# Performance work log

Hardware: AMD Instinct MI355X
Metric: run time of the kernel (lower is better)

The kernel has to match this reference:

```python
import jax, jax.numpy as jnp
import numpy as np
from jax import lax

B, S, H, W = 64, 256, 512, 512


def _lstm_cell(x_t, h, c, Wih, Whh, bih, bhh):
    # PyTorch LSTMCell gate order: i, f, g, o
    g = x_t @ Wih.T + h @ Whh.T + bih + bhh  # [B, 4H]
    i, f, gg, o = jnp.split(g, 4, axis=-1)
    c_new = jax.nn.sigmoid(f) * c + jax.nn.sigmoid(i) * jnp.tanh(gg)
    h_new = jax.nn.sigmoid(o) * jnp.tanh(c_new)
    return h_new, c_new


def setup_inputs() -> dict:
    key = jax.random.key(0)
    ks = jax.random.split(key, 12)
    bnd = 1.0 / np.sqrt(H)
    u = lambda k, shape, b: jax.random.uniform(k, shape, jnp.float32, -b, b)
    return {
        "x": jax.random.normal(ks[0], (B, S, S), jnp.float32),
        "enc_Wih": u(ks[1], (4 * H, S), bnd),
        "enc_Whh": u(ks[2], (4 * H, H), bnd),
        "enc_bih": u(ks[3], (4 * H,), bnd),
        "enc_bhh": u(ks[4], (4 * H,), bnd),
        "dec_Wih": u(ks[5], (4 * H, S), bnd),
        "dec_Whh": u(ks[6], (4 * H, H), bnd),
        "dec_bih": u(ks[7], (4 * H,), bnd),
        "dec_bhh": u(ks[8], (4 * H,), bnd),
        "w1": u(ks[9], (W, H), 1.0 / np.sqrt(H)),
        "w2": u(ks[10], (W, H), 1.0 / np.sqrt(H)),
        "vt": u(ks[11], (W,), 1.0 / np.sqrt(W)),
    }


def reference(x, enc_Wih, enc_Whh, enc_bih, enc_bhh,
              dec_Wih, dec_Whh, dec_bih, dec_bhh, w1, w2, vt):
    xs = x.transpose(1, 0, 2)  # [S, B, S] time-major

    # ---- encoder LSTM (zero initial state, PyTorch default) ----
    def enc_step(carry, x_t):
        h, c = carry
        h, c = _lstm_cell(x_t, h, c, enc_Wih, enc_Whh, enc_bih, enc_bhh)
        return (h, c), h

    h0 = jnp.zeros((B, H), x.dtype)
    (hT, cT), enc_out = lax.scan(enc_step, (h0, h0), xs)  # enc_out: [S, B, H]

    # loop-invariant W1 projection of encoder outputs
    e1 = jnp.einsum('sbh,wh->sbw', enc_out, w1)  # [S, B, W]

    # ---- decoder: hidden updates each step; cell stays at cT (faithful to source) ----
    def dec_step(h, x_t):
        h_new, _ = _lstm_cell(x_t, h, cT, dec_Wih, dec_Whh, dec_bih, dec_bhh)
        att = jnp.tanh(e1 + (h_new @ w2.T)[None, :, :])   # [S, B, W]
        scores = jnp.einsum('sbw,w->sb', att, vt)          # [S, B]
        lp = jax.nn.log_softmax(scores.T, axis=-1)         # [B, S]
        return h_new, lp

    _, probs = lax.scan(dec_step, hT, xs)  # [S_dec, B, S]
    return probs.transpose(1, 0, 2)        # [B, S_dec, S]
```

## Files before the change

kernel.cpp:

```cpp
#include <hip/hip_runtime.h>
#include <cmath>

__device__ __forceinline__ float sigm(float x) { return 1.0f / (1.0f + __expf(-x)); }

__global__ __launch_bounds__(256) void transpose_w(const float* __restrict__ in,
                                                   float* __restrict__ outT, int K) {
  __shared__ float tile[32][33];
  int tx = threadIdx.x & 31, ty = threadIdx.x >> 5;
  int k0 = blockIdx.x * 32;
  int j0 = blockIdx.y * 32;
#pragma unroll
  for (int i = 0; i < 32; i += 8)
    tile[ty + i][tx] = in[(size_t)(j0 + ty + i) * K + k0 + tx];
  __syncthreads();
#pragma unroll
  for (int i = 0; i < 32; i += 8)
    outT[(size_t)(k0 + ty + i) * 2048 + j0 + tx] = tile[tx][ty + i];
}

__device__ __forceinline__ void gemv_j(const float4* __restrict__ A4,
                                       const float4* __restrict__ W4, int j, int kqx,
                                       int kq, int jlo, int jhi, int b0, int b1,
                                       float (&o0)[8], float (&o1)[8]) {
  int qa = (j << 3) + kqx;
  float4 a04 = A4[b0 * 192 + qa];
  float4 a14 = A4[b1 * 192 + qa];
  int wr = ((j << 3) + kq) << 2;
  float a0v[4] = {a04.x, a04.y, a04.z, a04.w};
  float a1v[4] = {a14.x, a14.y, a14.z, a14.w};
#pragma unroll
  for (int i = 0; i < 4; ++i) {
    float4 wlo = W4[(wr + i) * 8 + jlo];
    float4 whi = W4[(wr + i) * 8 + jhi];
    o0[0] = fmaf(a0v[i], wlo.x, o0[0]);
    o0[1] = fmaf(a0v[i], wlo.y, o0[1]);
    o0[2] = fmaf(a0v[i], wlo.z, o0[2]);
    o0[3] = fmaf(a0v[i], wlo.w, o0[3]);
    o0[4] = fmaf(a0v[i], whi.x, o0[4]);
    o0[5] = fmaf(a0v[i], whi.y, o0[5]);
    o0[6] = fmaf(a0v[i], whi.z, o0[6]);
    o0[7] = fmaf(a0v[i], whi.w, o0[7]);
    o1[0] = fmaf(a1v[i], wlo.x, o1[0]);
    o1[1] = fmaf(a1v[i], wlo.y, o1[1]);
    o1[2] = fmaf(a1v[i], wlo.z, o1[2]);
    o1[3] = fmaf(a1v[i], wlo.w, o1[3]);
    o1[4] = fmaf(a1v[i], whi.x, o1[4]);
    o1[5] = fmaf(a1v[i], whi.y, o1[5]);
    o1[6] = fmaf(a1v[i], whi.z, o1[6]);
    o1[7] = fmaf(a1v[i], whi.w, o1[7]);
  }
}

__global__ __launch_bounds__(256, 1) void lstm_chain(
    const float* __restrict__ WT, const float* __restrict__ x,
    const float* __restrict__ bih, const float* __restrict__ bhh,
    float* __restrict__ HBUF,
    float* __restrict__ Cst,
    unsigned int* __restrict__ flg,
    int is_enc) {
  extern __shared__ float lds[];
  float4* W4 = (float4*)lds;
  float4* A4 = (float4*)(lds + 24576);
  float* gates = lds + 24576 + 12288;
  const int bg = blockIdx.x >> 6, ng = blockIdx.x & 63;
  const int tid = threadIdx.x;
  unsigned int* myflag = flg + (size_t)(bg * 64 + ng) * 32;
  unsigned int* dom = flg + (size_t)bg * 64 * 32;

#pragma unroll
  for (int r = 0; r < 24; ++r) {
    int idx = tid + 256 * r;
    int k = idx >> 3, j = idx & 7;
    float4 v =
        *(const float4*)(WT + (size_t)k * 2048 + (j >> 1) * 512 + ng * 8 + (j & 1) * 4);
    W4[k * 8 + (j ^ ((k >> 2) & 7))] = v;
  }
  float bi_i = 0.f, bi_f = 0.f, bi_g = 0.f, bi_o = 0.f, creg = 0.f;
  if (tid < 128) {
    int b = tid >> 3, n8 = tid & 7;
    int n_g = ng * 8 + n8;
    bi_i = bih[n_g] + bhh[n_g];
    bi_f = bih[512 + n_g] + bhh[512 + n_g];
    bi_g = bih[1024 + n_g] + bhh[1024 + n_g];
    bi_o = bih[1536 + n_g] + bhh[1536 + n_g];
    if (!is_enc) creg = Cst[(size_t)(bg * 16 + b) * 512 + n_g];
  }
#pragma unroll
  for (int r = 0; r < 8; ++r) {
    int idx = tid + 256 * r;
    int b = idx >> 7, q = idx & 127;
    float4 v;
    if (is_enc)
      v = make_float4(0.f, 0.f, 0.f, 0.f);
    else
      v = *(const float4*)(HBUF + ((size_t)(255 * 64) + bg * 16 + b) * 512 + 4 * q);
    A4[b * 192 + (q ^ ((b >> 1) & 7))] = v;
  }
#pragma unroll
  for (int r = 0; r < 4; ++r) {
    int idx = tid + 256 * r;
    int b = idx >> 6, q = idx & 63;
    float4 v = *(const float4*)(x + ((size_t)(bg * 16 + b) * 256 + 0) * 256 + 4 * q);
    A4[b * 192 + ((128 + q) ^ ((b >> 1) & 7))] = v;
  }
  __syncthreads();

  const int w = tid >> 6;
  const int lane = tid & 63;
  const int kq = lane >> 3, b8 = lane & 7;
  const int b0 = 2 * b8, b1 = b0 + 1;
  const int jlo = (2 * w) ^ kq, jhi = (2 * w + 1) ^ kq;
  const int kqx = kq ^ b8;

  for (int t = 0; t < 256; ++t) {
    float acc0[8], acc1[8];
#pragma unroll
    for (int g = 0; g < 8; ++g) { acc0[g] = 0.f; acc1[g] = 0.f; }
#pragma unroll 2
    for (int j = 0; j < 24; ++j)
      gemv_j(A4, W4, j, kqx, kq, jlo, jhi, b0, b1, acc0, acc1);
#pragma unroll
    for (int d = 8; d <= 32; d <<= 1) {
#pragma unroll
      for (int g = 0; g < 8; ++g) {
        acc0[g] += __shfl_xor(acc0[g], d, 64);
        acc1[g] += __shfl_xor(acc1[g], d, 64);
      }
    }
    if (kq == 0) {
#pragma unroll
      for (int g = 0; g < 8; ++g) {
        gates[b0 * 40 + w * 8 + g] = acc0[g];
        gates[b1 * 40 + w * 8 + g] = acc1[g];
      }
    }
    __syncthreads();
    if (tid < 128) {
      int b = tid >> 3, n8 = tid & 7;
      float pi = gates[b * 40 + n8] + bi_i;
      float pf = gates[b * 40 + 8 + n8] + bi_f;
      float pg = gates[b * 40 + 16 + n8] + bi_g;
      float po = gates[b * 40 + 24 + n8] + bi_o;
      float ig = sigm(pi), fg = sigm(pf), gg = tanhf(pg), og = sigm(po);
      float cn = fmaf(fg, creg, ig * gg);
      if (is_enc) creg = cn;
      float hn = og * tanhf(cn);
      float* hp = HBUF + ((size_t)t * 64 + bg * 16 + b) * 512 + ng * 8 + n8;
      __hip_atomic_store(hp, hn, __ATOMIC_RELAXED, __HIP_MEMORY_SCOPE_AGENT);
      if (is_enc && t == 255) Cst[(size_t)(bg * 16 + b) * 512 + ng * 8 + n8] = cn;
    }
    if (t == 255) break;
    asm volatile("s_waitcnt vmcnt(0)" ::: "memory");
    __syncthreads();
    if (tid == 0)
      __hip_atomic_store(myflag, (unsigned)(t + 1), __ATOMIC_RELAXED,
                         __HIP_MEMORY_SCOPE_AGENT);
    asm volatile("" ::: "memory");
#pragma unroll
    for (int r = 0; r < 4; ++r) {
      int idx = tid + 256 * r;
      int b = idx >> 6, q = idx & 63;
      float4 v =
          *(const float4*)(x + ((size_t)(bg * 16 + b) * 256 + (t + 1)) * 256 + 4 * q);
      A4[b * 192 + ((128 + q) ^ ((b >> 1) & 7))] = v;
    }
    if (tid < 64) {
      const unsigned tgt = (unsigned)(t + 1);
      unsigned int* fp = dom + (size_t)tid * 32;
      while (true) {
        unsigned v = __hip_atomic_load(fp, __ATOMIC_RELAXED, __HIP_MEMORY_SCOPE_AGENT);
        if (__all((int)(v >= tgt))) break;
        __builtin_amdgcn_s_sleep(1);
      }
    }
    __syncthreads();
    const float4* hb = (const float4*)(HBUF + (size_t)t * 64 * 512);
#pragma unroll
    for (int r = 0; r < 8; ++r) {
      int idx = tid + 256 * r;
      int b = idx >> 7, q = idx & 127;
      float4 v = hb[(size_t)(bg * 16 + b) * 128 + q];
      A4[b * 192 + (q ^ ((b >> 1) & 7))] = v;
    }
    __syncthreads();
  }
}

__global__ __launch_bounds__(256) void gemm_fp32(const float* __restrict__ A,
                                                 const float* __restrict__ W,
                                                 float* __restrict__ C, int N, int K) {
  __shared__ float As[16 * 132];
  __shared__ float Ws[16 * 132];
  int tid = threadIdx.x;
  int n0 = blockIdx.x * 128, m0 = blockIdx.y * 128;
  int row = tid >> 1;
  int kbase = (tid & 1) * 8;
  const float* ap = A + (size_t)(m0 + row) * K;
  const float* wp = W + (size_t)(n0 + row) * K;
  int ty = tid >> 4, tx = tid & 15;
  float acc[8][8];
#pragma unroll
  for (int i = 0; i < 8; ++i)
#pragma unroll
    for (int j = 0; j < 8; ++j) acc[i][j] = 0.f;

  for (int kt = 0; kt < K; kt += 16) {
    float4 va0 = *(const float4*)(ap + kt + kbase);
    float4 va1 = *(const float4*)(ap + kt + kbase + 4);
    float4 vw0 = *(const float4*)(wp + kt + kbase);
    float4 vw1 = *(const float4*)(wp + kt + kbase + 4);
    __syncthreads();
    As[(kbase + 0) * 132 + row] = va0.x;
    As[(kbase + 1) * 132 + row] = va0.y;
    As[(kbase + 2) * 132 + row] = va0.z;
    As[(kbase + 3) * 132 + row] = va0.w;
    As[(kbase + 4) * 132 + row] = va1.x;
    As[(kbase + 5) * 132 + row] = va1.y;
    As[(kbase + 6) * 132 + row] = va1.z;
    As[(kbase + 7) * 132 + row] = va1.w;
    Ws[(kbase + 0) * 132 + row] = vw0.x;
    Ws[(kbase + 1) * 132 + row] = vw0.y;
    Ws[(kbase + 2) * 132 + row] = vw0.z;
    Ws[(kbase + 3) * 132 + row] = vw0.w;
    Ws[(kbase + 4) * 132 + row] = vw1.x;
    Ws[(kbase + 5) * 132 + row] = vw1.y;
    Ws[(kbase + 6) * 132 + row] = vw1.z;
    Ws[(kbase + 7) * 132 + row] = vw1.w;
    __syncthreads();
#pragma unroll
    for (int kk = 0; kk < 16; ++kk) {
      float4 a0 = *(const float4*)&As[kk * 132 + ty * 8];
      float4 a1 = *(const float4*)&As[kk * 132 + ty * 8 + 4];
      float4 w0 = *(const float4*)&Ws[kk * 132 + tx * 8];
      float4 w1 = *(const float4*)&Ws[kk * 132 + tx * 8 + 4];
      float av[8] = {a0.x, a0.y, a0.z, a0.w, a1.x, a1.y, a1.z, a1.w};
      float wv[8] = {w0.x, w0.y, w0.z, w0.w, w1.x, w1.y, w1.z, w1.w};
#pragma unroll
      for (int i = 0; i < 8; ++i)
#pragma unroll
        for (int j = 0; j < 8; ++j) acc[i][j] = fmaf(av[i], wv[j], acc[i][j]);
    }
  }
#pragma unroll
  for (int i = 0; i < 8; ++i) {
    float* cp = C + (size_t)(m0 + ty * 8 + i) * N + n0 + tx * 8;
    *(float4*)cp = make_float4(acc[i][0], acc[i][1], acc[i][2], acc[i][3]);
    *(float4*)(cp + 4) = make_float4(acc[i][4], acc[i][5], acc[i][6], acc[i][7]);
  }
}

__global__ __launch_bounds__(256) void scorer(const float* __restrict__ E1,
                                              const float* __restrict__ H2,
                                              const float* __restrict__ vt,
                                              float* __restrict__ out) {
  extern __shared__ float smem[];
  float* e1s = smem;
  float* h2s = smem + 8256;
  int tid = threadIdx.x;
  int sx = blockIdx.x;
  int b = blockIdx.y;
#pragma unroll
  for (int j = 0; j < 8; ++j) {
    int idx = tid + 256 * j;
    int r = idx >> 7, c4 = idx & 127;
    float4 v = *(const float4*)(E1 + ((size_t)(sx * 16 + r) * 64 + b) * 512 + c4 * 4);
    *(float4*)&e1s[r * 516 + c4 * 4] = v;
  }
  int tl = tid >> 4, sl = tid & 15;
  for (int tt = 0; tt < 16; ++tt) {
    __syncthreads();
#pragma unroll
    for (int j = 0; j < 8; ++j) {
      int idx = tid + 256 * j;
      int r = idx >> 7, c4 = idx & 127;
      float4 v = *(const float4*)(H2 + ((size_t)(tt * 16 + r) * 64 + b) * 512 + c4 * 4);
      *(float4*)&h2s[r * 516 + c4 * 4] = v;
    }
    __syncthreads();
    float acc = 0.f;
    const float* ep = &e1s[sl * 516];
    const float* hp = &h2s[tl * 516];
#pragma unroll 8
    for (int w4 = 0; w4 < 128; ++w4) {
      float4 a = *(const float4*)(ep + w4 * 4);
      float4 h = *(const float4*)(hp + w4 * 4);
      float4 vv = *(const float4*)(vt + w4 * 4);
      float x0 = a.x + h.x, x1 = a.y + h.y, x2 = a.z + h.z, x3 = a.w + h.w;
      float t0 = fmaf(-2.f, __builtin_amdgcn_rcpf(__expf(x0 + x0) + 1.f), 1.f);
      float t1 = fmaf(-2.f, __builtin_amdgcn_rcpf(__expf(x1 + x1) + 1.f), 1.f);
      float t2 = fmaf(-2.f, __builtin_amdgcn_rcpf(__expf(x2 + x2) + 1.f), 1.f);
      float t3 = fmaf(-2.f, __builtin_amdgcn_rcpf(__expf(x3 + x3) + 1.f), 1.f);
      acc = fmaf(t0, vv.x, acc);
      acc = fmaf(t1, vv.y, acc);
      acc = fmaf(t2, vv.z, acc);
      acc = fmaf(t3, vv.w, acc);
    }
    out[((size_t)b * 256 + tt * 16 + tl) * 256 + sx * 16 + sl] = acc;
  }
}

__global__ __launch_bounds__(256) void logsoftmax_kernel(float* __restrict__ out) {
  __shared__ float red[256];
  int tid = threadIdx.x;
  float* row = out + (size_t)blockIdx.x * 256;
  float v = row[tid];
  red[tid] = v;
  __syncthreads();
  for (int off = 128; off > 0; off >>= 1) {
    if (tid < off) red[tid] = fmaxf(red[tid], red[tid + off]);
    __syncthreads();
  }
  float mx = red[0];
  __syncthreads();
  red[tid] = __expf(v - mx);
  __syncthreads();
  for (int off = 128; off > 0; off >>= 1) {
    if (tid < off) red[tid] += red[tid + off];
    __syncthreads();
  }
  float lse = logf(red[0]);
  row[tid] = v - mx - lse;
}

extern "C" void kernel_launch(void* const* d_in, const int* in_sizes, int n_in,
                              void* d_out, int out_size, void* d_ws, size_t ws_size,
                              hipStream_t stream) {
  (void)in_sizes; (void)n_in; (void)out_size; (void)ws_size;
  const float* x = (const float*)d_in[0];
  const float* eWih = (const float*)d_in[1];
  const float* eWhh = (const float*)d_in[2];
  const float* ebih = (const float*)d_in[3];
  const float* ebhh = (const float*)d_in[4];
  const float* dWih = (const float*)d_in[5];
  const float* dWhh = (const float*)d_in[6];
  const float* dbih = (const float*)d_in[7];
  const float* dbhh = (const float*)d_in[8];
  const float* w1 = (const float*)d_in[9];
  const float* w2 = (const float*)d_in[10];
  const float* vt = (const float*)d_in[11];
  float* out = (float*)d_out;
  float* ws = (float*)d_ws;

  float* E1 = ws;
  float* H2 = E1 + 8388608ull;
  float* HBUF = H2 + 8388608ull;
  float* WTe = HBUF + 8388608ull;
  float* WTd = WTe + 1572864ull;
  float* Cst = WTd + 1572864ull;
  unsigned int* FLG = (unsigned int*)(Cst + 32768ull);

  const unsigned ldsB = (24576 + 12288 + 640) * 4;
  const unsigned scorerLds = 2 * 16 * 516 * 4;

  hipMemsetAsync(FLG, 0, 16384 * sizeof(unsigned int), stream);
  transpose_w<<<dim3(16, 64), 256, 0, stream>>>(eWhh, WTe, 512);
  transpose_w<<<dim3(8, 64), 256, 0, stream>>>(eWih, WTe + 512 * 2048, 256);
  transpose_w<<<dim3(16, 64), 256, 0, stream>>>(dWhh, WTd, 512);
  transpose_w<<<dim3(8, 64), 256, 0, stream>>>(dWih, WTd + 512 * 2048, 256);

  {
    const float* a0 = WTe; const float* a1 = x; const float* a2 = ebih;
    const float* a3 = ebhh; float* a4 = HBUF; float* a5 = Cst;
    unsigned int* a6 = FLG; int a7 = 1;
    void* args[] = {&a0, &a1, &a2, &a3, &a4, &a5, &a6, &a7};
    hipLaunchCooperativeKernel((const void*)lstm_chain, dim3(256), dim3(256), args,
                               ldsB, stream);
  }
  gemm_fp32<<<dim3(4, 128), 256, 0, stream>>>(HBUF, w1, E1, 512, 512);
  {
    const float* a0 = WTd; const float* a1 = x; const float* a2 = dbih;
    const float* a3 = dbhh; float* a4 = HBUF; float* a5 = Cst;
    unsigned int* a6 = FLG + 8192; int a7 = 0;
    void* args[] = {&a0, &a1, &a2, &a3, &a4, &a5, &a6, &a7};
    hipLaunchCooperativeKernel((const void*)lstm_chain, dim3(256), dim3(256), args,
                               ldsB, stream);
  }
  gemm_fp32<<<dim3(4, 128), 256, 0, stream>>>(HBUF, w2, H2, 512, 512);
  scorer<<<dim3(16, 64), 256, scorerLds, stream>>>(E1, H2, vt, out);
  logsoftmax_kernel<<<16384, 256, 0, stream>>>(out);
}
```

Baseline: 4.056 ms.

## Stream pre-swizzled LSTM weights from global memory instead of LDS

```diff
diff --git a/kernel.cpp b/kernel.cpp
--- a/kernel.cpp
+++ b/kernel.cpp
@@ -3,19 +3,46 @@
 
 __device__ __forceinline__ float sigm(float x) { return 1.0f / (1.0f + __expf(-x)); }
 
-__global__ __launch_bounds__(256) void transpose_w(const float* __restrict__ in,
-                                                   float* __restrict__ outT, int K) {
-  __shared__ float tile[32][33];
-  int tx = threadIdx.x & 31, ty = threadIdx.x >> 5;
-  int k0 = blockIdx.x * 32;
-  int j0 = blockIdx.y * 32;
-#pragma unroll
-  for (int i = 0; i < 32; i += 8)
-    tile[ty + i][tx] = in[(size_t)(j0 + ty + i) * K + k0 + tx];
-  __syncthreads();
-#pragma unroll
-  for (int i = 0; i < 32; i += 8)
-    outT[(size_t)(k0 + ty + i) * 2048 + j0 + tx] = tile[tx][ty + i];
+__global__ __launch_bounds__(256) void prep_w(const float* __restrict__ Wih,
+                                              const float* __restrict__ Whh,
+                                              float* __restrict__ Wg) {
+  extern __shared__ float sm[];
+  float* sh = sm;
+  float* sx = sm + 16384;
+  int ng = blockIdx.x, tid = threadIdx.x;
+  for (int idx = tid; idx < 4096; idx += 256) {
+    int r = idx >> 7, q = idx & 127;
+    int row = (r >> 3) * 512 + ng * 8 + ((r >> 2) & 1) * 4 + (r & 3);
+    *(float4*)&sh[r * 512 + q * 4] = *(const float4*)(Whh + (size_t)row * 512 + q * 4);
+  }
+  for (int idx = tid; idx < 2048; idx += 256) {
+    int r = idx >> 6, q = idx & 63;
+    int row = (r >> 3) * 512 + ng * 8 + ((r >> 2) & 1) * 4 + (r & 3);
+    *(float4*)&sx[r * 256 + q * 4] = *(const float4*)(Wih + (size_t)row * 256 + q * 4);
+  }
+  __syncthreads();
+  for (int o = tid; o < 6144; o += 256) {
+    int kq = o & 7, c = (o >> 3) & 1, i = (o >> 4) & 3;
+    int jw = o >> 6;
+    int w = jw / 24, j = jw - w * 24;
+    int k = (j * 8 + kq) * 4 + i;
+    int rb = w * 8 + c * 4;
+    float4 v;
+    if (k < 512) {
+      v.x = sh[(rb + 0) * 512 + k];
+      v.y = sh[(rb + 1) * 512 + k];
+      v.z = sh[(rb + 2) * 512 + k];
+      v.w = sh[(rb + 3) * 512 + k];
+    } else {
+      int kk = k - 512;
+      v.x = sx[(rb + 0) * 256 + kk];
+      v.y = sx[(rb + 1) * 256 + kk];
+      v.z = sx[(rb + 2) * 256 + kk];
+      v.w = sx[(rb + 3) * 256 + kk];
+    }
+    int slot = (k << 3) + ((2 * w + c) ^ kq);
+    ((float4*)Wg)[(size_t)ng * 6144 + slot] = v;
+  }
 }
 
 __device__ __forceinline__ void gemv_j(const float4* __restrict__ A4,
@@ -52,29 +79,20 @@
 }
 
 __global__ __launch_bounds__(256, 1) void lstm_chain(
-    const float* __restrict__ WT, const float* __restrict__ x,
+    const float* __restrict__ WG, const float* __restrict__ x,
     const float* __restrict__ bih, const float* __restrict__ bhh,
     float* __restrict__ HBUF,
     float* __restrict__ Cst,
     unsigned int* __restrict__ flg,
     int is_enc) {
   extern __shared__ float lds[];
-  float4* W4 = (float4*)lds;
-  float4* A4 = (float4*)(lds + 24576);
-  float* gates = lds + 24576 + 12288;
+  float4* A4 = (float4*)lds;
+  float* gates = lds + 12288;
   const int bg = blockIdx.x >> 6, ng = blockIdx.x & 63;
   const int tid = threadIdx.x;
   unsigned int* myflag = flg + (size_t)(bg * 64 + ng) * 32;
   unsigned int* dom = flg + (size_t)bg * 64 * 32;
 
-#pragma unroll
-  for (int r = 0; r < 24; ++r) {
-    int idx = tid + 256 * r;
-    int k = idx >> 3, j = idx & 7;
-    float4 v =
-        *(const float4*)(WT + (size_t)k * 2048 + (j >> 1) * 512 + ng * 8 + (j & 1) * 4);
-    W4[k * 8 + (j ^ ((k >> 2) & 7))] = v;
-  }
   float bi_i = 0.f, bi_f = 0.f, bi_g = 0.f, bi_o = 0.f, creg = 0.f;
   if (tid < 128) {
     int b = tid >> 3, n8 = tid & 7;
@@ -111,6 +129,7 @@
   const int b0 = 2 * b8, b1 = b0 + 1;
   const int jlo = (2 * w) ^ kq, jhi = (2 * w + 1) ^ kq;
   const int kqx = kq ^ b8;
+  const float4* W4 = (const float4*)WG + (size_t)ng * 6144;
 
   for (int t = 0; t < 256; ++t) {
     float acc0[8], acc1[8];
@@ -344,22 +363,21 @@
   float* E1 = ws;
   float* H2 = E1 + 8388608ull;
   float* HBUF = H2 + 8388608ull;
-  float* WTe = HBUF + 8388608ull;
-  float* WTd = WTe + 1572864ull;
-  float* Cst = WTd + 1572864ull;
+  float* WGe = HBUF + 8388608ull;
+  float* WGd = WGe + 1572864ull;
+  float* Cst = WGd + 1572864ull;
   unsigned int* FLG = (unsigned int*)(Cst + 32768ull);
 
-  const unsigned ldsB = (24576 + 12288 + 640) * 4;
+  const unsigned ldsB = (12288 + 640) * 4;
+  const unsigned prepLds = (16384 + 8192) * 4;
   const unsigned scorerLds = 2 * 16 * 516 * 4;
 
   hipMemsetAsync(FLG, 0, 16384 * sizeof(unsigned int), stream);
-  transpose_w<<<dim3(16, 64), 256, 0, stream>>>(eWhh, WTe, 512);
-  transpose_w<<<dim3(8, 64), 256, 0, stream>>>(eWih, WTe + 512 * 2048, 256);
-  transpose_w<<<dim3(16, 64), 256, 0, stream>>>(dWhh, WTd, 512);
-  transpose_w<<<dim3(8, 64), 256, 0, stream>>>(dWih, WTd + 512 * 2048, 256);
+  prep_w<<<dim3(64), 256, prepLds, stream>>>(eWih, eWhh, WGe);
+  prep_w<<<dim3(64), 256, prepLds, stream>>>(dWih, dWhh, WGd);
 
   {
-    const float* a0 = WTe; const float* a1 = x; const float* a2 = ebih;
+    const float* a0 = WGe; const float* a1 = x; const float* a2 = ebih;
     const float* a3 = ebhh; float* a4 = HBUF; float* a5 = Cst;
     unsigned int* a6 = FLG; int a7 = 1;
     void* args[] = {&a0, &a1, &a2, &a3, &a4, &a5, &a6, &a7};
@@ -368,7 +386,7 @@
   }
   gemm_fp32<<<dim3(4, 128), 256, 0, stream>>>(HBUF, w1, E1, 512, 512);
   {
-    const float* a0 = WTd; const float* a1 = x; const float* a2 = dbih;
+    const float* a0 = WGd; const float* a1 = x; const float* a2 = dbih;
     const float* a3 = dbhh; float* a4 = HBUF; float* a5 = Cst;
     unsigned int* a6 = FLG + 8192; int a7 = 0;
     void* args[] = {&a0, &a1, &a2, &a3, &a4, &a5, &a6, &a7};
```

Measured after the change: 5.472 ms. 34.9% more time.
